# Performance work log

Hardware: AMD Instinct MI355X
Metric: run time of the kernel (lower is better)

## Reference

```python
import jax, jax.numpy as jnp
import numpy as np

T = 256   # time steps
F = 64    # features per step
H = 32    # LSTM hidden size
FORGET_BIAS = 1.0  # TF LSTMCell default


def setup_inputs() -> dict:
    key = jax.random.key(0)
    k1, k2, k3 = jax.random.split(key, 3)
    B = 16384
    x = jax.random.normal(k1, (B, T * F), dtype=jnp.float32)
    W_lstm = jax.random.normal(k2, (F + H, 4 * H), dtype=jnp.float32) * 0.1
    b_lstm = jnp.zeros((4 * H,), dtype=jnp.float32)
    W_dense = jax.random.normal(k3, (H, 1), dtype=jnp.float32) * 0.1
    b_dense = jnp.zeros((1,), dtype=jnp.float32)
    return {"x": x, "W_lstm": W_lstm, "b_lstm": b_lstm,
            "W_dense": W_dense, "b_dense": b_dense}


def reference(x, W_lstm, b_lstm, W_dense, b_dense):
    B = x.shape[0]
    # [B, T*F] -> [T, B, F] for scan over time
    xs = x.reshape(B, T, F).transpose(1, 0, 2)

    def step(carry, x_t):
        c, h = carry
        # TF LSTMCell: concat([inputs, h]) @ kernel + bias, gate order i, j, f, o
        gates = jnp.concatenate([x_t, h], axis=-1) @ W_lstm + b_lstm
        i, j, f, o = jnp.split(gates, 4, axis=-1)
        c_new = c * jax.nn.sigmoid(f + FORGET_BIAS) + jax.nn.sigmoid(i) * jnp.tanh(j)
        h_new = jnp.tanh(c_new) * jax.nn.sigmoid(o)
        return (c_new, h_new), None

    c0 = jnp.zeros((B, H), dtype=x.dtype)
    h0 = jnp.zeros((B, H), dtype=x.dtype)
    (c_T, h_T), _ = jax.lax.scan(step, (c0, h0), xs)

    # dense(1) + ELU on the final hidden state, then flatten like predict()
    out = jax.nn.elu(h_T @ W_dense + b_dense)
    return out.reshape(-1)
```

## Files before the change

kernel.cpp:

```cpp
#include <hip/hip_runtime.h>
#include <stdint.h>

#define T_STEPS 256
#define F_IN 64
#define L2E 1.44269504f

typedef __bf16 bf16x8 __attribute__((ext_vector_type(8)));
typedef float f32x4 __attribute__((ext_vector_type(4)));
typedef uint32_t u32;
typedef uint32_t u32x2 __attribute__((ext_vector_type(2)));
typedef uint32_t u32x4 __attribute__((ext_vector_type(4)));

#define GLDS16(gp, lp)                                                         \
    __builtin_amdgcn_global_load_lds(                                          \
        (const __attribute__((address_space(1))) unsigned int*)(gp),           \
        (__attribute__((address_space(3))) unsigned int*)(lp), 16, 0, 0)

static __device__ __forceinline__ u32 pk2(float lo, float hi) {
    unsigned short a = __builtin_bit_cast(unsigned short, (__bf16)lo);
    unsigned short b = __builtin_bit_cast(unsigned short, (__bf16)hi);
    return (u32)a | ((u32)b << 16);
}

__global__ __launch_bounds__(128, 2)
void lstm_fused(const float* __restrict__ x,
                const float* __restrict__ Wl,
                const float* __restrict__ bl,
                const float* __restrict__ Wd,
                const float* __restrict__ bd,
                float* __restrict__ out)
{
    __shared__ __align__(16) float  xs[4][1024];
    __shared__ __align__(16) __bf16 hf[2][64][8];

    const int lane = threadIdx.x & 63;
    const int wid  = threadIdx.x >> 6;
    const int cl   = lane & 15;
    const int g4   = lane >> 4;
    const int rowBase = blockIdx.x * 16;

    const float gsc[4] = {-L2E, -2.0f * L2E, -L2E, -L2E};

    bf16x8 wfrag[3][4];
#pragma unroll
    for (int kc = 0; kc < 3; ++kc) {
#pragma unroll
        for (int qi = 0; qi < 4; ++qi) {
            bf16x8 v;
#pragma unroll
            for (int j = 0; j < 8; ++j)
                v[j] = (__bf16)(gsc[qi] * Wl[(kc * 32 + g4 * 8 + j) * 128 + (2 * qi + wid) * 16 + cl]);
            wfrag[kc][qi] = v;
        }
    }

    f32x4 biasf[4];
#pragma unroll
    for (int qi = 0; qi < 4; ++qi) {
#pragma unroll
        for (int r = 0; r < 4; ++r) {
            const int gate = (2 * qi + wid) * 16 + g4 * 4 + r;
            biasf[qi][r] = gsc[qi] * (bl[gate] + (qi == 2 ? 1.0f : 0.0f));
        }
    }
    const float bd0 = bd[0];
    const f32x4 wdA = *(const f32x4*)(Wd + g4 * 8);
    const f32x4 wdB = *(const f32x4*)(Wd + g4 * 8 + 4);

    const float* gbase = x + (size_t)(rowBase + (lane >> 2)) * (size_t)(T_STEPS * F_IN)
                           + (size_t)(((lane & 3) ^ ((lane >> 3) & 3)) * 4);

    if (threadIdx.x < 64)
        *reinterpret_cast<u32x4*>(&hf[0][threadIdx.x][0]) = u32x4{0u, 0u, 0u, 0u};

    {
        const int phase = (blockIdx.x >> 8) & 3;
#pragma unroll 1
        for (int i = 0; i < phase; ++i) __builtin_amdgcn_s_sleep(10);
    }

    asm volatile("s_waitcnt vmcnt(0)" ::: "memory");
    __builtin_amdgcn_sched_barrier(0);

#pragma unroll
    for (int s = 0; s < 3; ++s) {
        const float* gp = gbase + s * F_IN + wid * 32;
        GLDS16(gp,      &xs[s][wid * 512]);
        GLDS16(gp + 16, &xs[s][wid * 512 + 256]);
    }

    asm volatile("s_waitcnt vmcnt(4) lgkmcnt(0)" ::: "memory");
    __builtin_amdgcn_sched_barrier(0);
    __builtin_amdgcn_s_barrier();
    __builtin_amdgcn_sched_barrier(0);

    const int swz = (cl >> 1) & 3;
    const int c0  = ((g4 & 1) * 2)     ^ swz;
    const int c1  = ((g4 & 1) * 2 + 1) ^ swz;
    const int kA  = (g4 >> 1) * 256 + cl * 16;
    const int kB  = kA + 512;

    const int tT = (2 * wid + (g4 >> 1)) * 16 + cl;
    const int e0 = (g4 & 1) * 4;

    float c_st[4] = {0.f, 0.f, 0.f, 0.f};

    f32x4 accx[4];
#define XGATES(SLOT) do {                                                      \
    const float* sl = &xs[SLOT][0];                                            \
    f32x4 xr0 = *(const f32x4*)(sl + kA + c0 * 4);                             \
    f32x4 xr1 = *(const f32x4*)(sl + kA + c1 * 4);                             \
    f32x4 xr2 = *(const f32x4*)(sl + kB + c0 * 4);                             \
    f32x4 xr3 = *(const f32x4*)(sl + kB + c1 * 4);                             \
    bf16x8 ax0, ax1;                                                           \
    _Pragma("unroll")                                                          \
    for (int j = 0; j < 4; ++j) {                                              \
        ax0[j]     = (__bf16)xr0[j];                                           \
        ax0[4 + j] = (__bf16)xr1[j];                                           \
        ax1[j]     = (__bf16)xr2[j];                                           \
        ax1[4 + j] = (__bf16)xr3[j];                                           \
    }                                                                          \
    _Pragma("unroll")                                                          \
    for (int qi = 0; qi < 4; ++qi) {                                           \
        f32x4 a = __builtin_amdgcn_mfma_f32_16x16x32_bf16(wfrag[0][qi], ax0, biasf[qi], 0, 0, 0); \
        accx[qi] = __builtin_amdgcn_mfma_f32_16x16x32_bf16(wfrag[1][qi], ax1, a, 0, 0, 0);        \
    }                                                                          \
} while (0)

    XGATES(0);

#define STEP(TT) do {                                                          \
    const int par = (TT) & 1;                                                  \
         \
    bf16x8 ah = *reinterpret_cast<const bf16x8*>(&hf[par][lane][0]);           \
    f32x4 acc[4];                                                              \
    __builtin_amdgcn_s_setprio(1);                                             \
    _Pragma("unroll")                                                          \
    for (int qi = 0; qi < 4; ++qi)                                             \
        acc[qi] = __builtin_amdgcn_mfma_f32_16x16x32_bf16(wfrag[2][qi], ah, accx[qi], 0, 0, 0); \
    __builtin_amdgcn_s_setprio(0);                                             \
    float hh[4];                                                               \
    _Pragma("unroll")                                                          \
    for (int r = 0; r < 4; ++r) {                                              \
        float I  = __builtin_amdgcn_exp2f(acc[0][r]);                          \
        float J  = __builtin_amdgcn_exp2f(acc[1][r]);                          \
        float Fv = __builtin_amdgcn_exp2f(acc[2][r]);                          \
        float O  = __builtin_amdgcn_exp2f(acc[3][r]);                          \
        float t3 = (1.0f + I) * (1.0f + J);                                    \
        float u  = 1.0f + Fv;                                                  \
        float np = __builtin_fmaf(J, 2.0f * L2E, -2.0f * L2E);                 \
        float r1 = __builtin_amdgcn_rcpf(t3 * u);                              \
        float num = __builtin_fmaf(c_st[r], t3, np * u);                       \
        float cp = num * r1;                                                   \
        float C  = __builtin_amdgcn_exp2f(cp);                                 \
        float r2 = __builtin_amdgcn_rcpf((1.0f + C) * (1.0f + O));             \
        hh[r] = (1.0f - C) * r2;                                               \
        c_st[r] = cp;                                                          \
    }                                                                          \
    *reinterpret_cast<u32x2*>(&hf[par ^ 1][tT][e0]) =                          \
        u32x2{pk2(hh[0], hh[1]), pk2(hh[2], hh[3])};                           \
            \
    const int tpf = ((TT) + 3 < T_STEPS) ? (TT) + 3 : T_STEPS - 1;             \
    const float* gp = gbase + tpf * F_IN + wid * 32;                           \
    GLDS16(gp,      &xs[((TT)+3) & 3][wid * 512]);                             \
    GLDS16(gp + 16, &xs[((TT)+3) & 3][wid * 512 + 256]);                       \
    asm volatile("s_waitcnt vmcnt(2)" ::: "memory");                           \
    __builtin_amdgcn_sched_barrier(0);                                         \
    const int tn = ((TT) + 1 < T_STEPS) ? (TT) + 1 : T_STEPS - 1;              \
    XGATES(tn & 3);                                                            \
                               \
    asm volatile("s_waitcnt lgkmcnt(0)" ::: "memory");                         \
    __builtin_amdgcn_sched_barrier(0);                                         \
    __builtin_amdgcn_s_barrier();                                              \
    __builtin_amdgcn_sched_barrier(0);                                         \
} while (0)

    for (int t = 0; t < T_STEPS; t += 4) {
        STEP(t);
        STEP(t + 1);
        STEP(t + 2);
        STEP(t + 3);
    }
#undef STEP
#undef XGATES

    asm volatile("s_waitcnt vmcnt(0)" ::: "memory");

    if (wid == 0) {
        bf16x8 hfin = *reinterpret_cast<const bf16x8*>(&hf[0][lane][0]);
        float v = 0.f;
#pragma unroll
        for (int j = 0; j < 4; ++j) {
            v = __builtin_fmaf((float)hfin[j],     wdA[j], v);
            v = __builtin_fmaf((float)hfin[4 + j], wdB[j], v);
        }
        v += __shfl_xor(v, 16, 64);
        v += __shfl_xor(v, 32, 64);
        if (lane < 16) {
            float z = v + bd0;
            out[rowBase + lane] = z > 0.f ? z : (__expf(z) - 1.0f);
        }
    }
}

extern "C" void kernel_launch(void* const* d_in, const int* in_sizes, int n_in,
                              void* d_out, int out_size, void* d_ws, size_t ws_size,
                              hipStream_t stream) {
    const float* x  = (const float*)d_in[0];
    const float* Wl = (const float*)d_in[1];
    const float* bl = (const float*)d_in[2];
    const float* Wd = (const float*)d_in[3];
    const float* bd = (const float*)d_in[4];
    float* out = (float*)d_out;

    const int rows = out_size;
    const int grid = (rows + 15) / 16;
    hipLaunchKernelGGL(lstm_fused, dim3(grid), dim3(128), 0, stream,
                       x, Wl, bl, Wd, bd, out);
}
```

Before: 240.8 us.

## Give each wavefront its own 16 rows and exchange hidden state via shuffles

Each wavefront now computes all eight gate quadrants for its own 16 batch rows, instead of two wavefronts splitting the gates of one 16-row tile. The hidden state moves between lanes with cross-lane shuffles rather than LDS writes followed by a block barrier, which removes the per-step barrier and LDS round trip. Each wavefront stages its own x slices with four async loads per step. The cost is doubled weight-fragment and accumulator registers per wave (launch bounds go to 256 threads, 1 block), eight shuffles per step, and removal of the staggered start sleep.

```diff
diff --git a/kernel.cpp b/kernel.cpp
--- a/kernel.cpp
+++ b/kernel.cpp
@@ -8,7 +8,6 @@
 typedef __bf16 bf16x8 __attribute__((ext_vector_type(8)));
 typedef float f32x4 __attribute__((ext_vector_type(4)));
 typedef uint32_t u32;
-typedef uint32_t u32x2 __attribute__((ext_vector_type(2)));
 typedef uint32_t u32x4 __attribute__((ext_vector_type(4)));
 
 #define GLDS16(gp, lp)                                                         \
@@ -22,7 +21,7 @@
     return (u32)a | ((u32)b << 16);
 }
 
-__global__ __launch_bounds__(128, 2)
+__global__ __launch_bounds__(256, 1)
 void lstm_fused(const float* __restrict__ x,
                 const float* __restrict__ Wl,
                 const float* __restrict__ bl,
@@ -30,69 +29,63 @@
                 const float* __restrict__ bd,
                 float* __restrict__ out)
 {
-    __shared__ __align__(16) float  xs[4][1024];
-    __shared__ __align__(16) __bf16 hf[2][64][8];
+    __shared__ __align__(16) float xs[4][4][1024];
 
     const int lane = threadIdx.x & 63;
     const int wid  = threadIdx.x >> 6;
     const int cl   = lane & 15;
     const int g4   = lane >> 4;
-    const int rowBase = blockIdx.x * 16;
-
-    const float gsc[4] = {-L2E, -2.0f * L2E, -L2E, -L2E};
-
-    bf16x8 wfrag[3][4];
+    const int rowBase = blockIdx.x * 64 + wid * 16;
+
+#define GSC(q) (((q) >> 1) == 1 ? -2.0f * L2E : -L2E)
+
+    bf16x8 wfrag[3][8];
 #pragma unroll
     for (int kc = 0; kc < 3; ++kc) {
 #pragma unroll
-        for (int qi = 0; qi < 4; ++qi) {
+        for (int q = 0; q < 8; ++q) {
             bf16x8 v;
 #pragma unroll
             for (int j = 0; j < 8; ++j)
-                v[j] = (__bf16)(gsc[qi] * Wl[(kc * 32 + g4 * 8 + j) * 128 + (2 * qi + wid) * 16 + cl]);
-            wfrag[kc][qi] = v;
+                v[j] = (__bf16)(GSC(q) * Wl[(kc * 32 + g4 * 8 + j) * 128 + q * 16 + cl]);
+            wfrag[kc][q] = v;
         }
     }
 
-    f32x4 biasf[4];
-#pragma unroll
-    for (int qi = 0; qi < 4; ++qi) {
+    f32x4 biasf[8];
+#pragma unroll
+    for (int q = 0; q < 8; ++q) {
 #pragma unroll
         for (int r = 0; r < 4; ++r) {
-            const int gate = (2 * qi + wid) * 16 + g4 * 4 + r;
-            biasf[qi][r] = gsc[qi] * (bl[gate] + (qi == 2 ? 1.0f : 0.0f));
+            const int gate = q * 16 + g4 * 4 + r;
+            biasf[q][r] = GSC(q) * (bl[gate] + ((q >> 1) == 2 ? 1.0f : 0.0f));
         }
     }
     const float bd0 = bd[0];
-    const f32x4 wdA = *(const f32x4*)(Wd + g4 * 8);
-    const f32x4 wdB = *(const f32x4*)(Wd + g4 * 8 + 4);
+    float wdl[4], wdh[4];
+#pragma unroll
+    for (int r = 0; r < 4; ++r) {
+        wdl[r] = Wd[4 * g4 + r];
+        wdh[r] = Wd[16 + 4 * g4 + r];
+    }
 
     const float* gbase = x + (size_t)(rowBase + (lane >> 2)) * (size_t)(T_STEPS * F_IN)
                            + (size_t)(((lane & 3) ^ ((lane >> 3) & 3)) * 4);
 
-    if (threadIdx.x < 64)
-        *reinterpret_cast<u32x4*>(&hf[0][threadIdx.x][0]) = u32x4{0u, 0u, 0u, 0u};
-
-    {
-        const int phase = (blockIdx.x >> 8) & 3;
-#pragma unroll 1
-        for (int i = 0; i < phase; ++i) __builtin_amdgcn_s_sleep(10);
-    }
-
     asm volatile("s_waitcnt vmcnt(0)" ::: "memory");
     __builtin_amdgcn_sched_barrier(0);
 
-#pragma unroll
-    for (int s = 0; s < 3; ++s) {
-        const float* gp = gbase + s * F_IN + wid * 32;
-        GLDS16(gp,      &xs[s][wid * 512]);
-        GLDS16(gp + 16, &xs[s][wid * 512 + 256]);
-    }
-
-    asm volatile("s_waitcnt vmcnt(4) lgkmcnt(0)" ::: "memory");
-    __builtin_amdgcn_sched_barrier(0);
-    __builtin_amdgcn_s_barrier();
-    __builtin_amdgcn_sched_barrier(0);
+#define STAGE(TT, SP) do {                                                     \
+    const float* gp = gbase + (TT) * F_IN;                                     \
+    GLDS16(gp,      &xs[wid][SP][0]);                                          \
+    GLDS16(gp + 16, &xs[wid][SP][256]);                                        \
+    GLDS16(gp + 32, &xs[wid][SP][512]);                                        \
+    GLDS16(gp + 48, &xs[wid][SP][768]);                                        \
+} while (0)
+
+    STAGE(0, 0);
+    STAGE(1, 1);
+    STAGE(2, 2);
 
     const int swz = (cl >> 1) & 3;
     const int c0  = ((g4 & 1) * 2)     ^ swz;
@@ -100,14 +93,38 @@
     const int kA  = (g4 >> 1) * 256 + cl * 16;
     const int kB  = kA + 512;
 
-    const int tT = (2 * wid + (g4 >> 1)) * 16 + cl;
-    const int e0 = (g4 & 1) * 4;
-
-    float c_st[4] = {0.f, 0.f, 0.f, 0.f};
-
-    f32x4 accx[4];
+    const int srcA = cl + 32 * (g4 & 1);
+    const int srcB = srcA + 16;
+    const int sel  = g4 >> 1;
+
+    f32x4 csl = {0.f, 0.f, 0.f, 0.f};
+    f32x4 csh = {0.f, 0.f, 0.f, 0.f};
+    f32x4 hlv, hhv;
+    u32x4 ahw = {0u, 0u, 0u, 0u};
+    f32x4 accx[8];
+
+#define CELL(AI, AJ, AF, AO, CS, HV) do {                                      \
+    _Pragma("unroll")                                                          \
+    for (int r = 0; r < 4; ++r) {                                              \
+        float I  = __builtin_amdgcn_exp2f((AI)[r]);                            \
+        float J  = __builtin_amdgcn_exp2f((AJ)[r]);                            \
+        float Fv = __builtin_amdgcn_exp2f((AF)[r]);                            \
+        float O  = __builtin_amdgcn_exp2f((AO)[r]);                            \
+        float t3 = (1.0f + I) * (1.0f + J);                                    \
+        float uu = 1.0f + Fv;                                                  \
+        float np = __builtin_fmaf(J, 2.0f * L2E, -2.0f * L2E);                 \
+        float r1 = __builtin_amdgcn_rcpf(t3 * uu);                             \
+        float nm = __builtin_fmaf((CS)[r], t3, np * uu);                       \
+        float cp = nm * r1;                                                    \
+        float C  = __builtin_amdgcn_exp2f(cp);                                 \
+        float r2 = __builtin_amdgcn_rcpf((1.0f + C) * (1.0f + O));             \
+        (HV)[r] = (1.0f - C) * r2;                                             \
+        (CS)[r] = cp;                                                          \
+    }                                                                          \
+} while (0)
+
 #define XGATES(SLOT) do {                                                      \
-    const float* sl = &xs[SLOT][0];                                            \
+    const float* sl = &xs[wid][SLOT][0];                                       \
     f32x4 xr0 = *(const f32x4*)(sl + kA + c0 * 4);                             \
     f32x4 xr1 = *(const f32x4*)(sl + kA + c1 * 4);                             \
     f32x4 xr2 = *(const f32x4*)(sl + kB + c0 * 4);                             \
@@ -121,58 +138,46 @@
         ax1[4 + j] = (__bf16)xr3[j];                                           \
     }                                                                          \
     _Pragma("unroll")                                                          \
-    for (int qi = 0; qi < 4; ++qi) {                                           \
-        f32x4 a = __builtin_amdgcn_mfma_f32_16x16x32_bf16(wfrag[0][qi], ax0, biasf[qi], 0, 0, 0); \
-        accx[qi] = __builtin_amdgcn_mfma_f32_16x16x32_bf16(wfrag[1][qi], ax1, a, 0, 0, 0);        \
+    for (int q = 0; q < 8; ++q) {                                              \
+        f32x4 a = __builtin_amdgcn_mfma_f32_16x16x32_bf16(wfrag[0][q], ax0, biasf[q], 0, 0, 0); \
+        accx[q] = __builtin_amdgcn_mfma_f32_16x16x32_bf16(wfrag[1][q], ax1, a, 0, 0, 0);        \
     }                                                                          \
 } while (0)
 
+    asm volatile("s_waitcnt vmcnt(8)" ::: "memory");
+    __builtin_amdgcn_sched_barrier(0);
     XGATES(0);
 
 #define STEP(TT) do {                                                          \
-    const int par = (TT) & 1;                                                  \
          \
-    bf16x8 ah = *reinterpret_cast<const bf16x8*>(&hf[par][lane][0]);           \
-    f32x4 acc[4];                                                              \
-    __builtin_amdgcn_s_setprio(1);                                             \
-    _Pragma("unroll")                                                          \
-    for (int qi = 0; qi < 4; ++qi)                                             \
-        acc[qi] = __builtin_amdgcn_mfma_f32_16x16x32_bf16(wfrag[2][qi], ah, accx[qi], 0, 0, 0); \
-    __builtin_amdgcn_s_setprio(0);                                             \
-    float hh[4];                                                               \
-    _Pragma("unroll")                                                          \
-    for (int r = 0; r < 4; ++r) {                                              \
-        float I  = __builtin_amdgcn_exp2f(acc[0][r]);                          \
-        float J  = __builtin_amdgcn_exp2f(acc[1][r]);                          \
-        float Fv = __builtin_amdgcn_exp2f(acc[2][r]);                          \
-        float O  = __builtin_amdgcn_exp2f(acc[3][r]);                          \
-        float t3 = (1.0f + I) * (1.0f + J);                                    \
-        float u  = 1.0f + Fv;                                                  \
-        float np = __builtin_fmaf(J, 2.0f * L2E, -2.0f * L2E);                 \
-        float r1 = __builtin_amdgcn_rcpf(t3 * u);                              \
-        float num = __builtin_fmaf(c_st[r], t3, np * u);                       \
-        float cp = num * r1;                                                   \
-        float C  = __builtin_amdgcn_exp2f(cp);                                 \
-        float r2 = __builtin_amdgcn_rcpf((1.0f + C) * (1.0f + O));             \
-        hh[r] = (1.0f - C) * r2;                                               \
-        c_st[r] = cp;                                                          \
-    }                                                                          \
-    *reinterpret_cast<u32x2*>(&hf[par ^ 1][tT][e0]) =                          \
-        u32x2{pk2(hh[0], hh[1]), pk2(hh[2], hh[3])};                           \
-            \
+    bf16x8 ah = __builtin_bit_cast(bf16x8, ahw);                               \
+    f32x4 acc[8];                                                              \
+    _Pragma("unroll")                                                          \
+    for (int q = 0; q < 8; ++q)                                                \
+        acc[q] = __builtin_amdgcn_mfma_f32_16x16x32_bf16(wfrag[2][q], ah, accx[q], 0, 0, 0); \
+    CELL(acc[0], acc[2], acc[4], acc[6], csl, hlv);                            \
+    CELL(acc[1], acc[3], acc[5], acc[7], csh, hhv);                            \
+               \
+    u32 W0 = pk2(hlv[0], hlv[1]);                                              \
+    u32 W1 = pk2(hlv[2], hlv[3]);                                              \
+    u32 W2 = pk2(hhv[0], hhv[1]);                                              \
+    u32 W3 = pk2(hhv[2], hhv[3]);                                              \
+               \
+    int A0 = __shfl((int)W0, srcA, 64), A1 = __shfl((int)W1, srcA, 64);        \
+    int A2 = __shfl((int)W2, srcA, 64), A3 = __shfl((int)W3, srcA, 64);        \
+    int B0 = __shfl((int)W0, srcB, 64), B1 = __shfl((int)W1, srcB, 64);        \
+    int B2 = __shfl((int)W2, srcB, 64), B3 = __shfl((int)W3, srcB, 64);        \
+    ahw[0] = (u32)(sel ? A2 : A0);                                             \
+    ahw[1] = (u32)(sel ? A3 : A1);                                             \
+    ahw[2] = (u32)(sel ? B2 : B0);                                             \
+    ahw[3] = (u32)(sel ? B3 : B1);                                             \
+           \
     const int tpf = ((TT) + 3 < T_STEPS) ? (TT) + 3 : T_STEPS - 1;             \
-    const float* gp = gbase + tpf * F_IN + wid * 32;                           \
-    GLDS16(gp,      &xs[((TT)+3) & 3][wid * 512]);                             \
-    GLDS16(gp + 16, &xs[((TT)+3) & 3][wid * 512 + 256]);                       \
-    asm volatile("s_waitcnt vmcnt(2)" ::: "memory");                           \
+    STAGE(tpf, ((TT) + 3) & 3);                                                \
+    asm volatile("s_waitcnt vmcnt(8)" ::: "memory");                           \
     __builtin_amdgcn_sched_barrier(0);                                         \
     const int tn = ((TT) + 1 < T_STEPS) ? (TT) + 1 : T_STEPS - 1;              \
     XGATES(tn & 3);                                                            \
-                               \
-    asm volatile("s_waitcnt lgkmcnt(0)" ::: "memory");                         \
-    __builtin_amdgcn_sched_barrier(0);                                         \
-    __builtin_amdgcn_s_barrier();                                              \
-    __builtin_amdgcn_sched_barrier(0);                                         \
 } while (0)
 
     for (int t = 0; t < T_STEPS; t += 4) {
@@ -183,23 +188,22 @@
     }
 #undef STEP
 #undef XGATES
+#undef CELL
+#undef STAGE
 
     asm volatile("s_waitcnt vmcnt(0)" ::: "memory");
 
-    if (wid == 0) {
-        bf16x8 hfin = *reinterpret_cast<const bf16x8*>(&hf[0][lane][0]);
-        float v = 0.f;
-#pragma unroll
-        for (int j = 0; j < 4; ++j) {
-            v = __builtin_fmaf((float)hfin[j],     wdA[j], v);
-            v = __builtin_fmaf((float)hfin[4 + j], wdB[j], v);
-        }
-        v += __shfl_xor(v, 16, 64);
-        v += __shfl_xor(v, 32, 64);
-        if (lane < 16) {
-            float z = v + bd0;
-            out[rowBase + lane] = z > 0.f ? z : (__expf(z) - 1.0f);
-        }
+    float v = 0.f;
+#pragma unroll
+    for (int r = 0; r < 4; ++r) {
+        v = __builtin_fmaf(hlv[r], wdl[r], v);
+        v = __builtin_fmaf(hhv[r], wdh[r], v);
+    }
+    v += __shfl_xor(v, 16, 64);
+    v += __shfl_xor(v, 32, 64);
+    if (lane < 16) {
+        float z = v + bd0;
+        out[rowBase + lane] = z > 0.f ? z : (__expf(z) - 1.0f);
     }
 }
 
@@ -214,7 +218,7 @@
     float* out = (float*)d_out;
 
     const int rows = out_size;
-    const int grid = (rows + 15) / 16;
-    hipLaunchKernelGGL(lstm_fused, dim3(grid), dim3(128), 0, stream,
+    const int grid = (rows + 63) / 64;
+    hipLaunchKernelGGL(lstm_fused, dim3(grid), dim3(256), 0, stream,
                        x, Wl, bl, Wd, bd, out);
 }
```

Result: no change. 240.1 us (-0.3%).
